# Performance work log

Measured on AMD Instinct MI355X. Metric: run time of the kernel, lower is better.

## Reference

```python
import jax, jax.numpy as jnp
import numpy as np

N_NODES = 100000


def gcn_conv(x, src, dst, dinv, W, b):
    # PyG GCNConv: h = D^-1/2 (A+I) D^-1/2 (x W) + b
    h = x @ W                                   # [N, out]
    norm = dinv[src] * dinv[dst]                # [E'] edge weights
    msg = norm[:, None] * h[src]                # gather + scale
    agg = jax.ops.segment_sum(msg, dst, num_segments=x.shape[0])
    return agg + b


def setup_inputs() -> dict:
    key = jax.random.key(0)
    ks = jax.random.split(key, 8)
    x = jax.random.normal(ks[0], (N_NODES, 64), dtype=jnp.float32)
    edge_index = jax.random.randint(ks[1], (2, 1600000), 0, N_NODES, dtype=jnp.int32)
    s = 0.1
    return {
        "x": x,
        "edge_index": edge_index,
        "W1": jax.random.normal(ks[2], (64, 64), dtype=jnp.float32) * s,
        "b1": jnp.zeros((64,), dtype=jnp.float32),
        "W2": jax.random.normal(ks[3], (64, 32), dtype=jnp.float32) * s,
        "b2": jnp.zeros((32,), dtype=jnp.float32),
        "W3": jax.random.normal(ks[4], (32, 2), dtype=jnp.float32) * s,
        "b3": jnp.zeros((2,), dtype=jnp.float32),
    }


def reference(x, edge_index, W1, b1, W2, b2, W3, b3):
    n = x.shape[0]
    loop = jnp.arange(n, dtype=edge_index.dtype)
    src = jnp.concatenate([edge_index[0], loop])  # add self-loops
    dst = jnp.concatenate([edge_index[1], loop])
    deg = jax.ops.segment_sum(jnp.ones_like(dst, dtype=x.dtype), dst, num_segments=n)
    dinv = jnp.where(deg > 0, jax.lax.rsqrt(jnp.maximum(deg, 1.0)), 0.0)
    h = jax.nn.relu(gcn_conv(x, src, dst, dinv, W1, b1))
    h = jax.nn.relu(gcn_conv(h, src, dst, dinv, W2, b2))
    return gcn_conv(h, src, dst, dinv, W3, b3)
```

## Files before the change

### kernel.cpp

```cpp
#include <hip/hip_runtime.h>
#include <hip/hip_fp16.h>

#define N_NODES 100000
#define N_EDGES 1600000
#define BSHIFT 9
#define NBUCK ((N_NODES + 511) / 512)
#define BCAP 12288

__global__ void bucket1_kernel(const int* __restrict__ src, const int* __restrict__ dst,
                               int* __restrict__ gbcount, int* __restrict__ bbuf, int E) {
    __shared__ int hcnt[NBUCK];
    __shared__ int hbase[NBUCK];
    int t = threadIdx.x;
    for (int i = t; i < NBUCK; i += 256) hcnt[i] = 0;
    __syncthreads();
    int e0 = blockIdx.x * 2048 + t;
    int ss[8], dd[8];
#pragma unroll
    for (int u = 0; u < 8; u++) {
        int e = e0 + u * 256;
        if (e < E) {
            ss[u] = src[e];
            dd[u] = dst[e];
            atomicAdd(&hcnt[dd[u] >> BSHIFT], 1);
        } else {
            dd[u] = -1;
        }
    }
    __syncthreads();
    for (int i = t; i < NBUCK; i += 256) {
        int c = hcnt[i];
        hbase[i] = c ? atomicAdd(&gbcount[i], c) : 0;
        hcnt[i] = 0;
    }
    __syncthreads();
#pragma unroll
    for (int u = 0; u < 8; u++) {
        if (dd[u] >= 0) {
            int bk = dd[u] >> BSHIFT;
            int r = atomicAdd(&hcnt[bk], 1);
            bbuf[(size_t)bk * BCAP + hbase[bk] + r] = ss[u] | ((dd[u] & 511) << 17);
        }
    }
}

__global__ void scan196_kernel(const int* __restrict__ gbcount, int* __restrict__ gbase,
                               int* __restrict__ rowptrN, int E) {
    __shared__ int s[256];
    int t = threadIdx.x;
    int v = (t < NBUCK) ? gbcount[t] : 0;
    s[t] = v;
    __syncthreads();
    for (int off = 1; off < 256; off <<= 1) {
        int u = (t >= off) ? s[t - off] : 0;
        __syncthreads();
        s[t] += u;
        __syncthreads();
    }
    if (t < NBUCK) gbase[t] = s[t] - v;
    if (t == 0) *rowptrN = E;
}

__global__ __launch_bounds__(512)
void bucket2_kernel(const int* __restrict__ bbuf, const int* __restrict__ gbcount,
                    const int* __restrict__ gbase, int* __restrict__ rowptr,
                    float* __restrict__ dinv, int* __restrict__ eidx, int N) {
    int b = blockIdx.x;
    int base_node = b << BSHIFT;
    int nn = min(512, N - base_node);
    int t = threadIdx.x;
    __shared__ int s[512];
    __shared__ int cur[512];
    s[t] = 0;
    __syncthreads();
    int sz = gbcount[b];
    const int* eb = bbuf + (size_t)b * BCAP;
    for (int j = t; j < sz; j += 512) atomicAdd(&s[((unsigned)eb[j]) >> 17], 1);
    __syncthreads();
    int myc = s[t];
    if (t < nn) dinv[base_node + t] = rsqrtf((float)myc + 1.0f);
    __syncthreads();
    for (int off = 1; off < 512; off <<= 1) {
        int u = (t >= off) ? s[t - off] : 0;
        __syncthreads();
        s[t] += u;
        __syncthreads();
    }
    int rp = gbase[b] + s[t] - myc;
    if (t < nn) rowptr[base_node + t] = rp;
    cur[t] = rp;
    __syncthreads();
    for (int j = t; j < sz; j += 512) {
        int e = eb[j];
        int pos = atomicAdd(&cur[((unsigned)e) >> 17], 1);
        eidx[pos] = e & 0x1FFFF;
    }
}

__global__ void sortrow_wave(const int* __restrict__ rowptr, int* __restrict__ eidx, int n) {
    int g = (blockIdx.x * blockDim.x + threadIdx.x) >> 6;
    int lane = threadIdx.x & 63;
    if (g >= n) return;
    int start = rowptr[g];
    int end = rowptr[g + 1];
    int len = end - start;
    if (len <= 1) return;

    if (len <= 64) {
        int v = (lane < len) ? eidx[start + lane] : 0x7fffffff;
#pragma unroll
        for (int k = 2; k <= 64; k <<= 1) {
#pragma unroll
            for (int j = k >> 1; j > 0; j >>= 1) {
                int partner = __shfl_xor(v, j, 64);
                bool up = ((lane & k) == 0);
                bool keepMin = (((lane & j) == 0) == up);
                int mn = min(v, partner), mx = max(v, partner);
                v = keepMin ? mn : mx;
            }
        }
        if (lane < len) eidx[start + lane] = v;
    } else if (lane == 0) {
        for (int i = start + 1; i < end; i++) {
            int key = eidx[i];
            int j = i - 1;
            while (j >= start && eidx[j] > key) { eidx[j + 1] = eidx[j]; j--; }
            eidx[j + 1] = key;
        }
    }
}

template <int FIN, int FOUT>
__global__ __launch_bounds__(256, 2)
void gemm_tiled(const float* __restrict__ in, const float* __restrict__ W,
                const float* __restrict__ dinv, __half* __restrict__ out, int n) {
    constexpr int CG = FOUT / 4;
    constexpr int RG = 256 / CG;
    constexpr int TR = RG * 4;
    constexpr int LDA = FIN + 4;
    __shared__ float sIn[TR * LDA];
    __shared__ float sW[FIN * FOUT];

    for (int i = threadIdx.x; i < FIN * FOUT / 4; i += 256)
        ((float4*)sW)[i] = ((const float4*)W)[i];

    int r0 = blockIdx.x * TR;
    for (int i = threadIdx.x; i < TR * FIN / 4; i += 256) {
        int rr = i / (FIN / 4);
        int cc = i % (FIN / 4);
        int gr = r0 + rr;
        float4 v = (gr < n) ? ((const float4*)in)[(size_t)gr * (FIN / 4) + cc]
                            : make_float4(0.f, 0.f, 0.f, 0.f);
        *(float4*)&sIn[rr * LDA + cc * 4] = v;
    }
    __syncthreads();

    int tc = threadIdx.x % CG;
    int tr = threadIdx.x / CG;
    int rbase = tr * 4, cbase = tc * 4;
    float acc[4][4] = {};

#pragma unroll 2
    for (int k = 0; k < FIN; k += 4) {
        float4 a[4], b[4];
#pragma unroll
        for (int i = 0; i < 4; i++) a[i] = *(float4*)&sIn[(rbase + i) * LDA + k];
#pragma unroll
        for (int kk = 0; kk < 4; kk++) b[kk] = *(float4*)&sW[(k + kk) * FOUT + cbase];
#pragma unroll
        for (int i = 0; i < 4; i++) {
            acc[i][0] += a[i].x * b[0].x + a[i].y * b[1].x + a[i].z * b[2].x + a[i].w * b[3].x;
            acc[i][1] += a[i].x * b[0].y + a[i].y * b[1].y + a[i].z * b[2].y + a[i].w * b[3].y;
            acc[i][2] += a[i].x * b[0].z + a[i].y * b[1].z + a[i].z * b[2].z + a[i].w * b[3].z;
            acc[i][3] += a[i].x * b[0].w + a[i].y * b[1].w + a[i].z * b[2].w + a[i].w * b[3].w;
        }
    }

#pragma unroll
    for (int i = 0; i < 4; i++) {
        int gr = r0 + rbase + i;
        if (gr < n) {
            float dv = dinv[gr];
            union { __half h[4]; uint2 u; } pk;
            pk.h[0] = __float2half_rn(dv * acc[i][0]);
            pk.h[1] = __float2half_rn(dv * acc[i][1]);
            pk.h[2] = __float2half_rn(dv * acc[i][2]);
            pk.h[3] = __float2half_rn(dv * acc[i][3]);
            *(uint2*)&out[(size_t)gr * FOUT + cbase] = pk.u;
        }
    }
}

template <int FIN, int FOUT, bool OUT_HALF>
__global__ __launch_bounds__(256, 4)
void agg_gemm_kernel(const int* __restrict__ eidx, const int* __restrict__ rowptr,
                     const float* __restrict__ dinv, const __half* __restrict__ h,
                     const float* __restrict__ bias, const float* __restrict__ W,
                     void* __restrict__ outv, int n) {
    constexpr int L = 8;
    constexpr int PH = FIN / L;
    constexpr int NODES = 256 / L;
    constexpr int SVS = FIN + 1;
    using vh = _Float16 __attribute__((ext_vector_type(PH)));
    __shared__ float sW[FIN * FOUT];
    __shared__ float sv[NODES * SVS];

    for (int i = threadIdx.x; i < FIN * FOUT / 4; i += 256)
        ((float4*)sW)[i] = ((const float4*)W)[i];

    int g = (blockIdx.x * blockDim.x + threadIdx.x) / L;
    int lane = threadIdx.x % L;
    int slot = threadIdx.x / L;
    float di = 0.f;

    if (g < n) {
        int j = rowptr[g];
        int end = rowptr[g + 1];
        di = dinv[g];
        const __half* hb = h + lane * PH;

        vh sf = *(const vh*)(hb + (size_t)g * FIN);

        float acc0[PH], acc1[PH];
#pragma unroll
        for (int q = 0; q < PH; q++) { acc0[q] = 0.f; acc1[q] = 0.f; }

        for (; j + 8 <= end; j += 8) {
            int s0 = eidx[j];
            int s1 = eidx[j + 1];
            int s2 = eidx[j + 2];
            int s3 = eidx[j + 3];
            int s4 = eidx[j + 4];
            int s5 = eidx[j + 5];
            int s6 = eidx[j + 6];
            int s7 = eidx[j + 7];
            vh v0 = *(const vh*)(hb + (size_t)s0 * FIN);
            vh v1 = *(const vh*)(hb + (size_t)s1 * FIN);
            vh v2 = *(const vh*)(hb + (size_t)s2 * FIN);
            vh v3 = *(const vh*)(hb + (size_t)s3 * FIN);
            vh v4 = *(const vh*)(hb + (size_t)s4 * FIN);
            vh v5 = *(const vh*)(hb + (size_t)s5 * FIN);
            vh v6 = *(const vh*)(hb + (size_t)s6 * FIN);
            vh v7 = *(const vh*)(hb + (size_t)s7 * FIN);
#pragma unroll
            for (int q = 0; q < PH; q++) {
                acc0[q] += (float)v0[q] + (float)v2[q];
                acc1[q] += (float)v1[q] + (float)v3[q];
                acc0[q] += (float)v4[q] + (float)v6[q];
                acc1[q] += (float)v5[q] + (float)v7[q];
            }
        }
        for (; j + 2 <= end; j += 2) {
            int s0 = eidx[j];
            int s1 = eidx[j + 1];
            vh v0 = *(const vh*)(hb + (size_t)s0 * FIN);
            vh v1 = *(const vh*)(hb + (size_t)s1 * FIN);
#pragma unroll
            for (int q = 0; q < PH; q++) { acc0[q] += (float)v0[q]; acc1[q] += (float)v1[q]; }
        }
        if (j < end) {
            vh v = *(const vh*)(hb + (size_t)eidx[j] * FIN);
#pragma unroll
            for (int q = 0; q < PH; q++) acc0[q] += (float)v[q];
        }

        float* svn = &sv[slot * SVS + lane * PH];
#pragma unroll
        for (int q = 0; q < PH; q++) {
            float v = di * ((acc0[q] + acc1[q]) + (float)sf[q]) + bias[lane * PH + q];
            svn[q] = fmaxf(v, 0.f);
        }
    }
    __syncthreads();

    if (g < n) {
        const float* vn = &sv[slot * SVS];
        if constexpr (OUT_HALF) {
            constexpr int PC = FOUT / L;
            float o[PC] = {};
            for (int k = 0; k < FIN; k++) {
                float vk = vn[k];
                float4 w = *(const float4*)&sW[k * FOUT + lane * PC];
                o[0] += vk * w.x; o[1] += vk * w.y; o[2] += vk * w.z; o[3] += vk * w.w;
            }
            union { __half h[4]; uint2 u; } pk;
#pragma unroll
            for (int q = 0; q < PC; q++) pk.h[q] = __float2half_rn(di * o[q]);
            *(uint2*)((__half*)outv + (size_t)g * FOUT + lane * PC) = pk.u;
        } else {
            if (lane < FOUT) {
                float o = 0.f;
                for (int k = 0; k < FIN; k++) o += vn[k] * sW[k * FOUT + lane];
                ((float*)outv)[(size_t)g * FOUT + lane] = di * o;
            }
        }
    }
}

__global__ void agg2_kernel(const int* __restrict__ eidx, const int* __restrict__ rowptr,
                            const float* __restrict__ dinv, const float* __restrict__ h,
                            const float* __restrict__ b, float* __restrict__ out, int n) {
    int g = blockIdx.x * blockDim.x + threadIdx.x;
    if (g >= n) return;
    const float2* h2 = (const float2*)h;
    int j = rowptr[g];
    int end = rowptr[g + 1];
    float di = dinv[g];
    float2 hs = h2[g];

    float2 a0 = {0.f, 0.f}, a1 = {0.f, 0.f}, a2 = {0.f, 0.f}, a3 = {0.f, 0.f};
    float2 a4 = {0.f, 0.f}, a5 = {0.f, 0.f}, a6 = {0.f, 0.f}, a7 = {0.f, 0.f};
    for (; j + 8 <= end; j += 8) {
        int s0 = eidx[j];
        int s1 = eidx[j + 1];
        int s2 = eidx[j + 2];
        int s3 = eidx[j + 3];
        int s4 = eidx[j + 4];
        int s5 = eidx[j + 5];
        int s6 = eidx[j + 6];
        int s7 = eidx[j + 7];
        float2 v0 = h2[s0]; float2 v1 = h2[s1];
        float2 v2 = h2[s2]; float2 v3 = h2[s3];
        float2 v4 = h2[s4]; float2 v5 = h2[s5];
        float2 v6 = h2[s6]; float2 v7 = h2[s7];
        a0.x += v0.x; a0.y += v0.y;  a1.x += v1.x; a1.y += v1.y;
        a2.x += v2.x; a2.y += v2.y;  a3.x += v3.x; a3.y += v3.y;
        a4.x += v4.x; a4.y += v4.y;  a5.x += v5.x; a5.y += v5.y;
        a6.x += v6.x; a6.y += v6.y;  a7.x += v7.x; a7.y += v7.y;
    }
    for (; j + 2 <= end; j += 2) {
        float2 v0 = h2[eidx[j]];
        float2 v1 = h2[eidx[j + 1]];
        a0.x += v0.x; a0.y += v0.y;
        a1.x += v1.x; a1.y += v1.y;
    }
    if (j < end) {
        float2 v = h2[eidx[j]];
        a2.x += v.x; a2.y += v.y;
    }
    float accx = ((a0.x + a1.x) + (a2.x + a3.x)) + ((a4.x + a5.x) + (a6.x + a7.x));
    float accy = ((a0.y + a1.y) + (a2.y + a3.y)) + ((a4.y + a5.y) + (a6.y + a7.y));
    float2 r;
    r.x = di * (accx + hs.x) + b[0];
    r.y = di * (accy + hs.y) + b[1];
    ((float2*)out)[g] = r;
}

extern "C" void kernel_launch(void* const* d_in, const int* in_sizes, int n_in,
                              void* d_out, int out_size, void* d_ws, size_t ws_size,
                              hipStream_t stream) {
    const float* x  = (const float*)d_in[0];
    const int* ei   = (const int*)d_in[1];
    const float* W1 = (const float*)d_in[2];
    const float* b1 = (const float*)d_in[3];
    const float* W2 = (const float*)d_in[4];
    const float* b2 = (const float*)d_in[5];
    const float* W3 = (const float*)d_in[6];
    const float* b3 = (const float*)d_in[7];
    float* out = (float*)d_out;

    const int N = N_NODES;
    const int E = N_EDGES;
    const int* src = ei;
    const int* dst = ei + E;

    char* p = (char*)d_ws;
    int*    rowptr  = (int*)p;            p += ((size_t)(N + 1) * 4 + 15) / 16 * 16;
    float*  dinv    = (float*)p;          p += ((size_t)N * 4 + 15) / 16 * 16;
    int*    gbcount = (int*)p;            p += ((size_t)NBUCK * 4 + 15) / 16 * 16;
    int*    gbase   = (int*)p;            p += ((size_t)NBUCK * 4 + 15) / 16 * 16;
    int*    eidx    = (int*)p;            p += (size_t)E * 4;
    __half* A1      = (__half*)p;         p += (size_t)N * 64 * 2;
    __half* A2      = (__half*)p;         p += (size_t)N * 32 * 2;
    float*  A3      = (float*)p;          p += (size_t)N * 2 * 4;
    int*    bbuf    = (int*)p;

    const int T = 256;

    hipMemsetAsync(gbcount, 0, NBUCK * sizeof(int), stream);
    bucket1_kernel<<<(E + 2047) / 2048, T, 0, stream>>>(src, dst, gbcount, bbuf, E);
    scan196_kernel<<<1, 256, 0, stream>>>(gbcount, gbase, rowptr + N, E);
    bucket2_kernel<<<NBUCK, 512, 0, stream>>>(bbuf, gbcount, gbase, rowptr, dinv, eidx, N);
    sortrow_wave<<<(N * 64 + T - 1) / T, T, 0, stream>>>(rowptr, eidx, N);

    gemm_tiled<64, 64><<<(N + 63) / 64, T, 0, stream>>>(x, W1, dinv, A1, N);

    agg_gemm_kernel<64, 32, true><<<(N + 31) / 32, T, 0, stream>>>(
        eidx, rowptr, dinv, A1, b1, W2, A2, N);

    agg_gemm_kernel<32, 2, false><<<(N + 31) / 32, T, 0, stream>>>(
        eidx, rowptr, dinv, A2, b2, W3, A3, N);

    agg2_kernel<<<(N + T - 1) / T, T, 0, stream>>>(eidx, rowptr, dinv, A3, b3, out, N);
}
```

Baseline: 271.1 us.

## Slice feature tables into 16-column panels for cache-local aggregation

The first GEMM now writes its fp16 output as column slices of 16 features, so each slice forms a compact n×16 table. Aggregation runs per slice, with the block index interleaving slices and node ranges, so each gather touches a smaller working set that fits better in cache. The fused aggregate+GEMM kernels are split into a slice aggregation kernel that writes fp32 activations, followed by a separate tiled GEMM for layer 2 and a small GEMM kernel for layer 3. This adds an fp32 intermediate round-trip and extra launches, in exchange for better gather locality; workspace buffers are aliased to hold the new intermediates.

```diff
diff --git a/kernel.cpp b/kernel.cpp
--- a/kernel.cpp
+++ b/kernel.cpp
@@ -176,6 +176,9 @@
         }
     }
 
+    int slice = cbase >> 4;
+    int cw = cbase & 15;
+    __half* obase = out + (size_t)slice * ((size_t)n * 16);
 #pragma unroll
     for (int i = 0; i < 4; i++) {
         int gr = r0 + rbase + i;
@@ -186,115 +189,108 @@
             pk.h[1] = __float2half_rn(dv * acc[i][1]);
             pk.h[2] = __float2half_rn(dv * acc[i][2]);
             pk.h[3] = __float2half_rn(dv * acc[i][3]);
-            *(uint2*)&out[(size_t)gr * FOUT + cbase] = pk.u;
-        }
-    }
-}
-
-template <int FIN, int FOUT, bool OUT_HALF>
+            *(uint2*)&obase[(size_t)gr * 16 + cw] = pk.u;
+        }
+    }
+}
+
+template <int SVSTR, int LOGX>
 __global__ __launch_bounds__(256, 4)
-void agg_gemm_kernel(const int* __restrict__ eidx, const int* __restrict__ rowptr,
-                     const float* __restrict__ dinv, const __half* __restrict__ h,
-                     const float* __restrict__ bias, const float* __restrict__ W,
-                     void* __restrict__ outv, int n) {
-    constexpr int L = 8;
-    constexpr int PH = FIN / L;
-    constexpr int NODES = 256 / L;
-    constexpr int SVS = FIN + 1;
-    using vh = _Float16 __attribute__((ext_vector_type(PH)));
-    __shared__ float sW[FIN * FOUT];
-    __shared__ float sv[NODES * SVS];
-
-    for (int i = threadIdx.x; i < FIN * FOUT / 4; i += 256)
-        ((float4*)sW)[i] = ((const float4*)W)[i];
-
-    int g = (blockIdx.x * blockDim.x + threadIdx.x) / L;
-    int lane = threadIdx.x % L;
-    int slot = threadIdx.x / L;
-    float di = 0.f;
-
-    if (g < n) {
-        int j = rowptr[g];
-        int end = rowptr[g + 1];
-        di = dinv[g];
-        const __half* hb = h + lane * PH;
-
-        vh sf = *(const vh*)(hb + (size_t)g * FIN);
-
-        float acc0[PH], acc1[PH];
-#pragma unroll
-        for (int q = 0; q < PH; q++) { acc0[q] = 0.f; acc1[q] = 0.f; }
-
-        for (; j + 8 <= end; j += 8) {
-            int s0 = eidx[j];
-            int s1 = eidx[j + 1];
-            int s2 = eidx[j + 2];
-            int s3 = eidx[j + 3];
-            int s4 = eidx[j + 4];
-            int s5 = eidx[j + 5];
-            int s6 = eidx[j + 6];
-            int s7 = eidx[j + 7];
-            vh v0 = *(const vh*)(hb + (size_t)s0 * FIN);
-            vh v1 = *(const vh*)(hb + (size_t)s1 * FIN);
-            vh v2 = *(const vh*)(hb + (size_t)s2 * FIN);
-            vh v3 = *(const vh*)(hb + (size_t)s3 * FIN);
-            vh v4 = *(const vh*)(hb + (size_t)s4 * FIN);
-            vh v5 = *(const vh*)(hb + (size_t)s5 * FIN);
-            vh v6 = *(const vh*)(hb + (size_t)s6 * FIN);
-            vh v7 = *(const vh*)(hb + (size_t)s7 * FIN);
-#pragma unroll
-            for (int q = 0; q < PH; q++) {
-                acc0[q] += (float)v0[q] + (float)v2[q];
-                acc1[q] += (float)v1[q] + (float)v3[q];
-                acc0[q] += (float)v4[q] + (float)v6[q];
-                acc1[q] += (float)v5[q] + (float)v7[q];
-            }
-        }
-        for (; j + 2 <= end; j += 2) {
-            int s0 = eidx[j];
-            int s1 = eidx[j + 1];
-            vh v0 = *(const vh*)(hb + (size_t)s0 * FIN);
-            vh v1 = *(const vh*)(hb + (size_t)s1 * FIN);
-#pragma unroll
-            for (int q = 0; q < PH; q++) { acc0[q] += (float)v0[q]; acc1[q] += (float)v1[q]; }
-        }
-        if (j < end) {
-            vh v = *(const vh*)(hb + (size_t)eidx[j] * FIN);
-#pragma unroll
-            for (int q = 0; q < PH; q++) acc0[q] += (float)v[q];
-        }
-
-        float* svn = &sv[slot * SVS + lane * PH];
-#pragma unroll
-        for (int q = 0; q < PH; q++) {
-            float v = di * ((acc0[q] + acc1[q]) + (float)sf[q]) + bias[lane * PH + q];
-            svn[q] = fmaxf(v, 0.f);
-        }
-    }
-    __syncthreads();
-
-    if (g < n) {
-        const float* vn = &sv[slot * SVS];
-        if constexpr (OUT_HALF) {
-            constexpr int PC = FOUT / L;
-            float o[PC] = {};
-            for (int k = 0; k < FIN; k++) {
-                float vk = vn[k];
-                float4 w = *(const float4*)&sW[k * FOUT + lane * PC];
-                o[0] += vk * w.x; o[1] += vk * w.y; o[2] += vk * w.z; o[3] += vk * w.w;
-            }
-            union { __half h[4]; uint2 u; } pk;
-#pragma unroll
-            for (int q = 0; q < PC; q++) pk.h[q] = __float2half_rn(di * o[q]);
-            *(uint2*)((__half*)outv + (size_t)g * FOUT + lane * PC) = pk.u;
-        } else {
-            if (lane < FOUT) {
-                float o = 0.f;
-                for (int k = 0; k < FIN; k++) o += vn[k] * sW[k * FOUT + lane];
-                ((float*)outv)[(size_t)g * FOUT + lane] = di * o;
-            }
-        }
-    }
+void agg_slice_kernel(const __half* __restrict__ tbl, const int* __restrict__ eidx,
+                      const int* __restrict__ rowptr, const float* __restrict__ dinv,
+                      const float* __restrict__ bias, float* __restrict__ sv, int n) {
+    constexpr int SF = 16;
+    constexpr int L = 2;
+    constexpr int NPB = 256 / L;
+    using vh = _Float16 __attribute__((ext_vector_type(8)));
+
+    int blk = blockIdx.x;
+    int slice = (blk & 7) >> LOGX;
+    int nb = ((blk >> 3) << LOGX) | (blk & ((1 << LOGX) - 1));
+    int g = nb * NPB + (int)(threadIdx.x / L);
+    if (g >= n) return;
+    int lane = threadIdx.x & (L - 1);
+
+    const __half* hb = tbl + (size_t)slice * ((size_t)n * SF) + lane * 8;
+    int j = rowptr[g];
+    int end = rowptr[g + 1];
+    float di = dinv[g];
+
+    float acc0[8], acc1[8];
+#pragma unroll
+    for (int q = 0; q < 8; q++) { acc0[q] = 0.f; acc1[q] = 0.f; }
+
+    for (; j + 8 <= end; j += 8) {
+        int s0 = eidx[j];
+        int s1 = eidx[j + 1];
+        int s2 = eidx[j + 2];
+        int s3 = eidx[j + 3];
+        int s4 = eidx[j + 4];
+        int s5 = eidx[j + 5];
+        int s6 = eidx[j + 6];
+        int s7 = eidx[j + 7];
+        vh v0 = *(const vh*)(hb + (size_t)s0 * SF);
+        vh v1 = *(const vh*)(hb + (size_t)s1 * SF);
+        vh v2 = *(const vh*)(hb + (size_t)s2 * SF);
+        vh v3 = *(const vh*)(hb + (size_t)s3 * SF);
+        vh v4 = *(const vh*)(hb + (size_t)s4 * SF);
+        vh v5 = *(const vh*)(hb + (size_t)s5 * SF);
+        vh v6 = *(const vh*)(hb + (size_t)s6 * SF);
+        vh v7 = *(const vh*)(hb + (size_t)s7 * SF);
+#pragma unroll
+        for (int q = 0; q < 8; q++) {
+            acc0[q] += (float)v0[q] + (float)v2[q];
+            acc1[q] += (float)v1[q] + (float)v3[q];
+            acc0[q] += (float)v4[q] + (float)v6[q];
+            acc1[q] += (float)v5[q] + (float)v7[q];
+        }
+    }
+    for (; j + 2 <= end; j += 2) {
+        int s0 = eidx[j];
+        int s1 = eidx[j + 1];
+        vh v0 = *(const vh*)(hb + (size_t)s0 * SF);
+        vh v1 = *(const vh*)(hb + (size_t)s1 * SF);
+#pragma unroll
+        for (int q = 0; q < 8; q++) { acc0[q] += (float)v0[q]; acc1[q] += (float)v1[q]; }
+    }
+    if (j < end) {
+        vh v = *(const vh*)(hb + (size_t)eidx[j] * SF);
+#pragma unroll
+        for (int q = 0; q < 8; q++) acc0[q] += (float)v[q];
+    }
+
+    vh sf_ = *(const vh*)(hb + (size_t)g * SF);
+    const float* bp = bias + slice * SF + lane * 8;
+    float r[8];
+#pragma unroll
+    for (int q = 0; q < 8; q++) {
+        float v = di * ((acc0[q] + acc1[q]) + (float)sf_[q]) + bp[q];
+        r[q] = fmaxf(v, 0.f);
+    }
+    float* op = sv + (size_t)g * SVSTR + slice * SF + lane * 8;
+    *(float4*)op = make_float4(r[0], r[1], r[2], r[3]);
+    *(float4*)(op + 4) = make_float4(r[4], r[5], r[6], r[7]);
+}
+
+__global__ void gemm3_kernel(const float* __restrict__ sv2, const float* __restrict__ W3,
+                             const float* __restrict__ dinv, float* __restrict__ A3, int n) {
+    __shared__ float sW[64];
+    if (threadIdx.x < 64) sW[threadIdx.x] = W3[threadIdx.x];
+    __syncthreads();
+    int g = blockIdx.x * 256 + threadIdx.x;
+    if (g >= n) return;
+    const float4* r = (const float4*)(sv2 + (size_t)g * 32);
+    float c0 = 0.f, c1 = 0.f;
+#pragma unroll
+    for (int k4 = 0; k4 < 8; k4++) {
+        float4 v = r[k4];
+        int k = k4 * 4;
+        c0 += v.x * sW[(k + 0) * 2] + v.y * sW[(k + 1) * 2] + v.z * sW[(k + 2) * 2] + v.w * sW[(k + 3) * 2];
+        c1 += v.x * sW[(k + 0) * 2 + 1] + v.y * sW[(k + 1) * 2 + 1] + v.z * sW[(k + 2) * 2 + 1] + v.w * sW[(k + 3) * 2 + 1];
+    }
+    float di = dinv[g];
+    float2 o; o.x = di * c0; o.y = di * c1;
+    ((float2*)A3)[g] = o;
 }
 
 __global__ void agg2_kernel(const int* __restrict__ eidx, const int* __restrict__ rowptr,
@@ -370,10 +366,12 @@
     int*    gbcount = (int*)p;            p += ((size_t)NBUCK * 4 + 15) / 16 * 16;
     int*    gbase   = (int*)p;            p += ((size_t)NBUCK * 4 + 15) / 16 * 16;
     int*    eidx    = (int*)p;            p += (size_t)E * 4;
-    __half* A1      = (__half*)p;         p += (size_t)N * 64 * 2;
     __half* A2      = (__half*)p;         p += (size_t)N * 32 * 2;
     float*  A3      = (float*)p;          p += (size_t)N * 2 * 4;
-    int*    bbuf    = (int*)p;
+    float*  SV1     = (float*)p;
+    int*    bbuf    = (int*)p;            p += (size_t)N * 64 * 4;
+    __half* A1      = (__half*)p;
+    float*  SV2     = (float*)p;
 
     const int T = 256;
 
@@ -385,11 +383,16 @@
 
     gemm_tiled<64, 64><<<(N + 63) / 64, T, 0, stream>>>(x, W1, dinv, A1, N);
 
-    agg_gemm_kernel<64, 32, true><<<(N + 31) / 32, T, 0, stream>>>(
-        eidx, rowptr, dinv, A1, b1, W2, A2, N);
-
-    agg_gemm_kernel<32, 2, false><<<(N + 31) / 32, T, 0, stream>>>(
-        eidx, rowptr, dinv, A2, b2, W3, A3, N);
+    int bps1 = (N + 127) / 128;
+    agg_slice_kernel<64, 1><<<(bps1 / 2) * 8, T, 0, stream>>>(
+        A1, eidx, rowptr, dinv, b1, SV1, N);
+
+    gemm_tiled<64, 32><<<(N + 127) / 128, T, 0, stream>>>(SV1, W2, dinv, A2, N);
+
+    agg_slice_kernel<32, 2><<<((bps1 + 3) / 4) * 8, T, 0, stream>>>(
+        A2, eidx, rowptr, dinv, b2, SV2, N);
+
+    gemm3_kernel<<<(N + 255) / 256, T, 0, stream>>>(SV2, W3, dinv, A3, N);
 
     agg2_kernel<<<(N + T - 1) / T, T, 0, stream>>>(eidx, rowptr, dinv, A3, b3, out, N);
 }
```

After: 299.7 us. +10.5%, slower.

## Fuse per-row edge sort into bucket2 using shared-memory staging

Applied to the files above, without the earlier changes.

Each bucket's edges are scattered into a shared-memory buffer instead of global eidx. Every row is then sorted there by wave-level bitonic sort, and the sorted bucket is written to global memory with coalesced stores. This drops the separate sortrow_wave launch and its global read-modify-write traffic. It costs about 48KB of LDS per block, which lowers occupancy of the 196-block bucket2 kernel. The self-loop feature load in the aggregation kernel is also moved after the neighbour loop, a minor register-pressure tweak.

```diff
diff --git a/kernel.cpp b/kernel.cpp
--- a/kernel.cpp
+++ b/kernel.cpp
@@ -70,10 +70,12 @@
     int nn = min(512, N - base_node);
     int t = threadIdx.x;
     __shared__ int s[512];
-    __shared__ int cur[512];
+    __shared__ int lcur[512];
+    __shared__ int loc[BCAP];
     s[t] = 0;
     __syncthreads();
     int sz = gbcount[b];
+    int gb = gbase[b];
     const int* eb = bbuf + (size_t)b * BCAP;
     for (int j = t; j < sz; j += 512) atomicAdd(&s[((unsigned)eb[j]) >> 17], 1);
     __syncthreads();
@@ -86,48 +88,48 @@
         s[t] += u;
         __syncthreads();
     }
-    int rp = gbase[b] + s[t] - myc;
-    if (t < nn) rowptr[base_node + t] = rp;
-    cur[t] = rp;
+    int lstart = s[t] - myc;
+    if (t < nn) rowptr[base_node + t] = gb + lstart;
+    lcur[t] = lstart;
     __syncthreads();
     for (int j = t; j < sz; j += 512) {
         int e = eb[j];
-        int pos = atomicAdd(&cur[((unsigned)e) >> 17], 1);
-        eidx[pos] = e & 0x1FFFF;
-    }
-}
-
-__global__ void sortrow_wave(const int* __restrict__ rowptr, int* __restrict__ eidx, int n) {
-    int g = (blockIdx.x * blockDim.x + threadIdx.x) >> 6;
-    int lane = threadIdx.x & 63;
-    if (g >= n) return;
-    int start = rowptr[g];
-    int end = rowptr[g + 1];
-    int len = end - start;
-    if (len <= 1) return;
-
-    if (len <= 64) {
-        int v = (lane < len) ? eidx[start + lane] : 0x7fffffff;
-#pragma unroll
-        for (int k = 2; k <= 64; k <<= 1) {
-#pragma unroll
-            for (int j = k >> 1; j > 0; j >>= 1) {
-                int partner = __shfl_xor(v, j, 64);
-                bool up = ((lane & k) == 0);
-                bool keepMin = (((lane & j) == 0) == up);
-                int mn = min(v, partner), mx = max(v, partner);
-                v = keepMin ? mn : mx;
-            }
-        }
-        if (lane < len) eidx[start + lane] = v;
-    } else if (lane == 0) {
-        for (int i = start + 1; i < end; i++) {
-            int key = eidx[i];
-            int j = i - 1;
-            while (j >= start && eidx[j] > key) { eidx[j + 1] = eidx[j]; j--; }
-            eidx[j + 1] = key;
-        }
-    }
+        int pos = atomicAdd(&lcur[((unsigned)e) >> 17], 1);
+        loc[pos] = e & 0x1FFFF;
+    }
+    __syncthreads();
+    int wid = t >> 6;
+    int lane = t & 63;
+    for (int r = wid; r < 512; r += 8) {
+        int end_l = s[r];
+        int st_l = (r == 0) ? 0 : s[r - 1];
+        int len = end_l - st_l;
+        if (len <= 1) continue;
+        if (len <= 64) {
+            int v = (lane < len) ? loc[st_l + lane] : 0x7fffffff;
+#pragma unroll
+            for (int k = 2; k <= 64; k <<= 1) {
+#pragma unroll
+                for (int j = k >> 1; j > 0; j >>= 1) {
+                    int partner = __shfl_xor(v, j, 64);
+                    bool up = ((lane & k) == 0);
+                    bool keepMin = (((lane & j) == 0) == up);
+                    int mn = min(v, partner), mx = max(v, partner);
+                    v = keepMin ? mn : mx;
+                }
+            }
+            if (lane < len) loc[st_l + lane] = v;
+        } else if (lane == 0) {
+            for (int i = st_l + 1; i < end_l; i++) {
+                int key = loc[i];
+                int j = i - 1;
+                while (j >= st_l && loc[j] > key) { loc[j + 1] = loc[j]; j--; }
+                loc[j + 1] = key;
+            }
+        }
+    }
+    __syncthreads();
+    for (int j = t; j < sz; j += 512) eidx[gb + j] = loc[j];
 }
 
 template <int FIN, int FOUT>
@@ -218,8 +220,6 @@
         int end = rowptr[g + 1];
         di = dinv[g];
         const __half* hb = h + lane * PH;
-
-        vh sf = *(const vh*)(hb + (size_t)g * FIN);
 
         float acc0[PH], acc1[PH];
 #pragma unroll
@@ -264,6 +264,7 @@
             for (int q = 0; q < PH; q++) acc0[q] += (float)v[q];
         }
 
+        vh sf = *(const vh*)(hb + (size_t)g * FIN);
         float* svn = &sv[slot * SVS + lane * PH];
 #pragma unroll
         for (int q = 0; q < PH; q++) {
@@ -381,7 +382,6 @@
     bucket1_kernel<<<(E + 2047) / 2048, T, 0, stream>>>(src, dst, gbcount, bbuf, E);
     scan196_kernel<<<1, 256, 0, stream>>>(gbcount, gbase, rowptr + N, E);
     bucket2_kernel<<<NBUCK, 512, 0, stream>>>(bbuf, gbcount, gbase, rowptr, dinv, eidx, N);
-    sortrow_wave<<<(N * 64 + T - 1) / T, T, 0, stream>>>(rowptr, eidx, N);
 
     gemm_tiled<64, 64><<<(N + 63) / 64, T, 0, stream>>>(x, W1, dinv, A1, N);
 
```

Measured after the change: 291.1 us. 1.07x slower.
